# Performance work log

Measured on AMD Instinct MI355X. Metric: run time of the kernel, lower is better.

## Reference

```python
import jax, jax.numpy as jnp
import numpy as np

H = 2048
NBINS = 256

def setup_inputs() -> dict:
    key = jax.random.key(0)
    k1, k2, k3, k4 = jax.random.split(key, 4)
    input_data = jax.random.uniform(k1, (1, 3, H, H), jnp.float32, -1.0, 1.0)
    target_data = jax.random.uniform(k2, (1, 3, H, H), jnp.float32, -1.0, 1.0)
    mask_src = (jax.random.uniform(k3, (1, 1, H, H)) > 0.5).astype(jnp.float32)
    mask_tar = (jax.random.uniform(k4, (1, 1, H, H)) > 0.5).astype(jnp.float32)
    return {"input_data": input_data, "target_data": target_data,
            "mask_src": mask_src, "mask_tar": mask_tar}


def _de_norm(x):
    # (x+1)/2 clamped to [0,1]
    return jnp.clip((x + 1.0) * 0.5, 0.0, 1.0)


def _masked_cdf(img, mask):
    # img: [3,H,W] in [0,255]; mask: [H,W] 0/1 weights.
    # Equivalent to np.histogram(masked_pixels, bins=256, range=(0,255)) per
    # channel followed by normalized cumsum: weighted bincount over all pixels.
    bins = jnp.clip(jnp.floor(img * (NBINS / 255.0)).astype(jnp.int32), 0, NBINS - 1)
    offs = bins + (jnp.arange(3, dtype=jnp.int32) * NBINS)[:, None, None]
    w = jnp.broadcast_to(mask, img.shape).reshape(-1)
    hist = jax.ops.segment_sum(w, offs.reshape(-1), num_segments=3 * NBINS)
    hist = hist.reshape(3, NBINS)
    cdf = jnp.cumsum(hist, axis=1)
    total = jnp.maximum(cdf[:, -1:], 1.0)  # number of masked pixels
    return cdf / total


def _cal_trans(dst_cdf, ref_cdf):
    # Faithful vectorization of PSGAN cal_trans: for i in 1..255, table[i] is
    # the first j in 1..255 with ref_cdf[j-1] <= dst_cdf[i] <= ref_cdf[j],
    # else i; table[0]=0, table[255]=255.
    j0 = jnp.searchsorted(ref_cdf, dst_cdf, side='left')
    cand = jnp.clip(j0, 1, NBINS - 1)
    ok = (ref_cdf[cand - 1] <= dst_cdf) & (ref_cdf[cand] >= dst_cdf)
    idx = jnp.arange(NBINS)
    table = jnp.where(ok, cand, idx)
    table = table.at[0].set(0).at[NBINS - 1].set(NBINS - 1)
    return table


def _histogram_loss(input_data, target_data, mask_src, mask_tar):
    inp = _de_norm(input_data)[0] * 255.0   # [3,H,W]
    tar = _de_norm(target_data)[0] * 255.0  # [3,H,W]
    ms = mask_src[0, 0]  # [H,W]
    mt = mask_tar[0, 0]
    input_masked = inp * ms
    target_masked = tar * mt

    cdf_dst = _masked_cdf(input_masked, ms)   # [3,256]
    cdf_ref = _masked_cdf(target_masked, mt)  # [3,256]
    tables = jax.vmap(_cal_trans)(cdf_dst, cdf_ref)  # [3,256] int

    # remap masked pixels through per-channel LUT (int() truncation)
    pix = jnp.clip(input_masked.astype(jnp.int32), 0, NBINS - 1)  # [3,H,W]
    matched = jnp.take_along_axis(tables, pix.reshape(3, -1), axis=1)
    matched = matched.reshape(input_masked.shape).astype(input_masked.dtype)
    input_match = jnp.where(ms[None] != 0, matched, input_masked)
    input_match = jax.lax.stop_gradient(input_match)  # to_var(requires_grad=False)

    return jnp.mean(jnp.abs(input_masked - input_match))


def reference(input_data, target_data, mask_src, mask_tar):
    return _histogram_loss(input_data, target_data, mask_src, mask_tar)
```

## Files before the change

kernel.cpp:

```cpp
#include <hip/hip_runtime.h>

#define HH 2048
#define NPIX (HH * HH)
#define NBINS 256
#define NQ (NPIX / 4)

#define GHIST_WORDS (6 * NBINS)
#define GCNT_WORDS  (3 * NBINS)
#define GFRAC_WORDS (3 * NBINS)
#define WS_ZERO_BYTES ((GHIST_WORDS + GCNT_WORDS + GFRAC_WORDS) * 4)

__device__ __forceinline__ float denorm255(float x) {
    return fminf(fmaxf((x + 1.0f) * 0.5f, 0.0f), 1.0f) * 255.0f;
}

__global__ __launch_bounds__(512) void fused_hist(
        const float* __restrict__ in, const float* __restrict__ tar,
        const float* __restrict__ ms, const float* __restrict__ mt,
        unsigned* __restrict__ ghist, unsigned* __restrict__ gcnt,
        float* __restrict__ gfrac) {
    __shared__ unsigned lhs[3 * NBINS];
    __shared__ unsigned lht[3 * NBINS];
    __shared__ unsigned lc [3 * NBINS];
    __shared__ float    lf [3 * NBINS];
    for (int i = threadIdx.x; i < 3 * NBINS; i += blockDim.x) {
        lhs[i] = 0u; lht[i] = 0u; lc[i] = 0u; lf[i] = 0.0f;
    }
    __syncthreads();

    const float BSCALE = 256.0f / 255.0f;
    const int stride = gridDim.x * blockDim.x;
    for (int idx = blockIdx.x * blockDim.x + threadIdx.x; idx < NQ; idx += stride) {
        float4 m4 = ((const float4*)ms)[idx];
        float4 t4 = ((const float4*)mt)[idx];
        float mv[4] = {m4.x, m4.y, m4.z, m4.w};
        float tv[4] = {t4.x, t4.y, t4.z, t4.w};
        #pragma unroll
        for (int ch = 0; ch < 3; ++ch) {
            float4 a = ((const float4*)(in  + (size_t)ch * NPIX))[idx];
            float4 b = ((const float4*)(tar + (size_t)ch * NPIX))[idx];
            float av[4] = {a.x, a.y, a.z, a.w};
            float bv[4] = {b.x, b.y, b.z, b.w};
            #pragma unroll
            for (int k = 0; k < 4; ++k) {
                if (mv[k] != 0.0f) {
                    float v = denorm255(av[k]);
                    int hb = min(max((int)floorf(v * BSCALE), 0), NBINS - 1);
                    atomicAdd(&lhs[ch * NBINS + hb], 1u);
                    int tb = min((int)v, NBINS - 1);
                    atomicAdd(&lc[ch * NBINS + tb], 1u);
                    atomicAdd(&lf[ch * NBINS + tb], v - (float)tb);
                }
                if (tv[k] != 0.0f) {
                    float v = denorm255(bv[k]);
                    int hb = min(max((int)floorf(v * BSCALE), 0), NBINS - 1);
                    atomicAdd(&lht[ch * NBINS + hb], 1u);
                }
            }
        }
    }
    __syncthreads();
    for (int i = threadIdx.x; i < 3 * NBINS; i += blockDim.x) {
        unsigned a = lhs[i]; if (a) atomicAdd(&ghist[i], a);
        unsigned b = lht[i]; if (b) atomicAdd(&ghist[3 * NBINS + i], b);
        unsigned c = lc[i];  if (c) atomicAdd(&gcnt[i], c);
        float    f = lf[i];  if (f != 0.0f) atomicAdd(&gfrac[i], f);
    }
}

__global__ __launch_bounds__(NBINS) void table_loss(
        const unsigned* __restrict__ ghist, const unsigned* __restrict__ gcnt,
        const float* __restrict__ gfrac, float* __restrict__ out) {
    __shared__ float cdf[6][NBINS];
    __shared__ float tot[6];
    const int t = threadIdx.x;
    #pragma unroll
    for (int j = 0; j < 6; ++j) cdf[j][t] = (float)ghist[j * NBINS + t];
    __syncthreads();
    #pragma unroll
    for (int off = 1; off < NBINS; off <<= 1) {
        float add[6];
        #pragma unroll
        for (int j = 0; j < 6; ++j) add[j] = (t >= off) ? cdf[j][t - off] : 0.0f;
        __syncthreads();
        #pragma unroll
        for (int j = 0; j < 6; ++j) cdf[j][t] += add[j];
        __syncthreads();
    }
    if (t < 6) tot[t] = fmaxf(cdf[t][NBINS - 1], 1.0f);
    __syncthreads();
    #pragma unroll
    for (int j = 0; j < 6; ++j) cdf[j][t] = cdf[j][t] / tot[j];
    __syncthreads();

    double lsum = 0.0;
    #pragma unroll
    for (int ch = 0; ch < 3; ++ch) {
        const float d = cdf[ch][t];
        const float* ref = cdf[3 + ch];
        int lo = 0, hi = NBINS;
        while (lo < hi) {
            int mid = (lo + hi) >> 1;
            if (ref[mid] < d) lo = mid + 1; else hi = mid;
        }
        int cand = min(max(lo, 1), NBINS - 1);
        int T = (ref[cand - 1] <= d && ref[cand] >= d) ? cand : t;
        if (t == 0) T = 0;
        if (t == NBINS - 1) T = NBINS - 1;

        const int b = t;
        const double c = (double)gcnt[ch * NBINS + t];
        const double F = (double)gfrac[ch * NBINS + t];
        lsum += (T <= b) ? (c * (double)(b - T) + F)
                         : (c * (double)(T - b) - F);
    }
    #pragma unroll
    for (int off = 32; off; off >>= 1) lsum += __shfl_down(lsum, off, 64);
    __shared__ double wsum[4];
    if ((t & 63) == 0) wsum[t >> 6] = lsum;
    __syncthreads();
    if (t == 0)
        out[0] = (float)((wsum[0] + wsum[1] + wsum[2] + wsum[3]) / (double)(3 * NPIX));
}

extern "C" void kernel_launch(void* const* d_in, const int* in_sizes, int n_in,
                              void* d_out, int out_size, void* d_ws, size_t ws_size,
                              hipStream_t stream) {
    const float* in  = (const float*)d_in[0];
    const float* tar = (const float*)d_in[1];
    const float* ms  = (const float*)d_in[2];
    const float* mt  = (const float*)d_in[3];
    float* out = (float*)d_out;

    unsigned* ghist = (unsigned*)d_ws;
    unsigned* gcnt  = ghist + GHIST_WORDS;
    float*    gfrac = (float*)(gcnt + GCNT_WORDS);

    hipMemsetAsync(d_ws, 0, WS_ZERO_BYTES, stream);
    fused_hist<<<512, 512, 0, stream>>>(in, tar, ms, mt, ghist, gcnt, gfrac);
    table_loss<<<1, NBINS, 0, stream>>>(ghist, gcnt, gfrac, out);
}
```

Before: 168.0 us.

## Pack count and fixed-point fraction into one 64-bit atomic; double grid

Replaces the separate per-bin count atomic and float fraction atomic with a single 64-bit integer atomic that holds the count in the high bits and a 22-bit fixed-point fraction sum in the low bits. This halves the LDS atomics on the source path and drops float atomics, which are likely emulated with compare-and-swap loops. The grid also grows from 512 to 1024 blocks and the launch bounds now request occupancy. The trade-off is quantization of the fraction sum and a risk of the fraction field overflowing into the count bits, since the field has 42 bits and the per-bin sums could be large.

Result: no change. 166.4 us (-0.9%).

```diff
diff --git a/kernel.cpp b/kernel.cpp
--- a/kernel.cpp
+++ b/kernel.cpp
@@ -6,29 +6,31 @@
 #define NQ (NPIX / 4)
 
 #define GHIST_WORDS (6 * NBINS)
-#define GCNT_WORDS  (3 * NBINS)
-#define GFRAC_WORDS (3 * NBINS)
-#define WS_ZERO_BYTES ((GHIST_WORDS + GCNT_WORDS + GFRAC_WORDS) * 4)
+#define GPK_WORDS   (3 * NBINS)
+#define WS_ZERO_BYTES (GHIST_WORDS * 4 + GPK_WORDS * 8)
+
+#define FRAC_BITS 22
+#define CNT_SHIFT 42
+#define FRAC_MASK ((1ULL << CNT_SHIFT) - 1)
 
 __device__ __forceinline__ float denorm255(float x) {
     return fminf(fmaxf((x + 1.0f) * 0.5f, 0.0f), 1.0f) * 255.0f;
 }
 
-__global__ __launch_bounds__(512) void fused_hist(
+__global__ __launch_bounds__(512, 8) void fused_hist(
         const float* __restrict__ in, const float* __restrict__ tar,
         const float* __restrict__ ms, const float* __restrict__ mt,
-        unsigned* __restrict__ ghist, unsigned* __restrict__ gcnt,
-        float* __restrict__ gfrac) {
+        unsigned* __restrict__ ghist, unsigned long long* __restrict__ gpk) {
     __shared__ unsigned lhs[3 * NBINS];
     __shared__ unsigned lht[3 * NBINS];
-    __shared__ unsigned lc [3 * NBINS];
-    __shared__ float    lf [3 * NBINS];
+    __shared__ unsigned long long lpk[3 * NBINS];
     for (int i = threadIdx.x; i < 3 * NBINS; i += blockDim.x) {
-        lhs[i] = 0u; lht[i] = 0u; lc[i] = 0u; lf[i] = 0.0f;
+        lhs[i] = 0u; lht[i] = 0u; lpk[i] = 0ull;
     }
     __syncthreads();
 
     const float BSCALE = 256.0f / 255.0f;
+    const float FSCALE = 4194304.0f;
     const int stride = gridDim.x * blockDim.x;
     for (int idx = blockIdx.x * blockDim.x + threadIdx.x; idx < NQ; idx += stride) {
         float4 m4 = ((const float4*)ms)[idx];
@@ -48,8 +50,9 @@
                     int hb = min(max((int)floorf(v * BSCALE), 0), NBINS - 1);
                     atomicAdd(&lhs[ch * NBINS + hb], 1u);
                     int tb = min((int)v, NBINS - 1);
-                    atomicAdd(&lc[ch * NBINS + tb], 1u);
-                    atomicAdd(&lf[ch * NBINS + tb], v - (float)tb);
+                    unsigned fr = (unsigned)((v - (float)tb) * FSCALE);
+                    atomicAdd(&lpk[ch * NBINS + tb],
+                              (1ULL << CNT_SHIFT) | (unsigned long long)fr);
                 }
                 if (tv[k] != 0.0f) {
                     float v = denorm255(bv[k]);
@@ -63,14 +66,14 @@
     for (int i = threadIdx.x; i < 3 * NBINS; i += blockDim.x) {
         unsigned a = lhs[i]; if (a) atomicAdd(&ghist[i], a);
         unsigned b = lht[i]; if (b) atomicAdd(&ghist[3 * NBINS + i], b);
-        unsigned c = lc[i];  if (c) atomicAdd(&gcnt[i], c);
-        float    f = lf[i];  if (f != 0.0f) atomicAdd(&gfrac[i], f);
+        unsigned long long p = lpk[i]; if (p) atomicAdd(&gpk[i], p);
     }
 }
 
 __global__ __launch_bounds__(NBINS) void table_loss(
-        const unsigned* __restrict__ ghist, const unsigned* __restrict__ gcnt,
-        const float* __restrict__ gfrac, float* __restrict__ out) {
+        const unsigned* __restrict__ ghist,
+        const unsigned long long* __restrict__ gpk,
+        float* __restrict__ out) {
     __shared__ float cdf[6][NBINS];
     __shared__ float tot[6];
     const int t = threadIdx.x;
@@ -109,8 +112,9 @@
         if (t == NBINS - 1) T = NBINS - 1;
 
         const int b = t;
-        const double c = (double)gcnt[ch * NBINS + t];
-        const double F = (double)gfrac[ch * NBINS + t];
+        const unsigned long long pk = gpk[ch * NBINS + t];
+        const double c = (double)(pk >> CNT_SHIFT);
+        const double F = (double)(pk & FRAC_MASK) * (1.0 / 4194304.0);
         lsum += (T <= b) ? (c * (double)(b - T) + F)
                          : (c * (double)(T - b) - F);
     }
@@ -133,10 +137,9 @@
     float* out = (float*)d_out;
 
     unsigned* ghist = (unsigned*)d_ws;
-    unsigned* gcnt  = ghist + GHIST_WORDS;
-    float*    gfrac = (float*)(gcnt + GCNT_WORDS);
+    unsigned long long* gpk = (unsigned long long*)((char*)d_ws + GHIST_WORDS * 4);
 
     hipMemsetAsync(d_ws, 0, WS_ZERO_BYTES, stream);
-    fused_hist<<<512, 512, 0, stream>>>(in, tar, ms, mt, ghist, gcnt, gfrac);
-    table_loss<<<1, NBINS, 0, stream>>>(ghist, gcnt, gfrac, out);
+    fused_hist<<<1024, 512, 0, stream>>>(in, tar, ms, mt, ghist, gpk);
+    table_loss<<<1, NBINS, 0, stream>>>(ghist, gpk, out);
 }
```
